# Performance work log

Hardware: AMD Instinct MI355X
Metric: run time of the kernel (lower is better)

Reference implementation:

```python
import jax, jax.numpy as jnp
import numpy as np

N = 200000          # nodes
G = 8192            # graphs (data.num_graphs)
NUM_RADIAL = 32
M_OUT = 85          # embedding_depth // 3 -> 85x1o


def setup_inputs() -> dict:
    key = jax.random.key(0)
    ks = jax.random.split(key, 24)
    f32 = jnp.float32
    def rn(k, shape, scale=1.0):
        return jax.random.normal(k, shape, dtype=f32) * scale
    inp = {}
    inp['pos'] = rn(ks[0], (N, 3))
    inp['z'] = jax.random.randint(ks[1], (N,), 0, 100)
    inp['batch'] = jnp.sort(jax.random.randint(ks[2], (N,), 0, G))
    inp['node_table'] = rn(ks[3], (100, 32))
    # MLP weights (fan-in scaled), biases zero
    inp['W_rbf0'] = rn(ks[4], (32, 64), 32 ** -0.5)
    inp['b_rbf0'] = jnp.zeros((64,), f32)
    inp['W_rbf1'] = rn(ks[5], (64, 64), 64 ** -0.5)
    inp['b_rbf1'] = jnp.zeros((64,), f32)
    inp['W_m0'] = rn(ks[6], (96, 64), 96 ** -0.5)
    inp['b_m0'] = jnp.zeros((64,), f32)
    inp['W_m1'] = rn(ks[7], (64, 64), 64 ** -0.5)
    inp['b_m1'] = jnp.zeros((64,), f32)
    inp['W_m2'] = rn(ks[8], (64, 64), 64 ** -0.5)
    inp['b_m2'] = jnp.zeros((64,), f32)
    # e3nn-style weights: N(0,1), path normalization applied in the math
    inp['w_tp0'] = rn(ks[9], (64, 64))   # 0e x 0e -> 0e
    inp['w_tp1'] = rn(ks[10], (64, 64))  # 0e x 1o -> 1o
    inp['w_tp2'] = rn(ks[11], (64, 32))  # 0e x 2e -> 2e
    inp['L0'] = rn(ks[12], (64, 64))     # o3.Linear 0e block
    inp['L1o'] = rn(ks[13], (64, 64))    # o3.Linear 1o block
    inp['L2e'] = rn(ks[14], (32, 32))    # o3.Linear 2e block
    inp['L_out'] = rn(ks[15], (64, 85))  # tl2: 64x1o -> 85x1o
    return inp


def _sph_harm(pos):
    # e3nn real spherical harmonics, normalize=False, normalization='component'
    x, y, z = pos[:, 0], pos[:, 1], pos[:, 2]
    sh0 = jnp.ones_like(x)                              # [N]     l=0
    sh1 = jnp.sqrt(3.0) * pos                           # [N,3]   l=1
    s15 = jnp.sqrt(15.0)
    s5 = jnp.sqrt(5.0)
    sh2 = jnp.stack([
        s15 * x * z,
        s15 * x * y,
        s5 * (y * y - 0.5 * (x * x + z * z)),
        s15 * y * z,
        0.5 * s15 * (z * z - x * x),
    ], axis=-1)                                          # [N,5]   l=2
    return sh0, sh1, sh2


def _forward(pos, z, batch, node_table, W_rbf0, b_rbf0, W_rbf1, b_rbf1,
             W_m0, b_m0, W_m1, b_m1, W_m2, b_m2,
             w_tp0, w_tp1, w_tp2, L0, L1o, L2e, L_out):
    sh0, sh1, sh2 = _sph_harm(pos)  # centroid is zeros

    # Gaussian RBF on |pos|, start=0 stop=1
    dist = jnp.linalg.norm(pos, axis=1)                  # [N]
    offsets = jnp.linspace(0.0, 1.0, NUM_RADIAL)
    coeff = -0.5 / (offsets[1] - offsets[0]) ** 2
    rbf = jnp.exp(coeff * (dist[:, None] - offsets) ** 2)  # [N,32]

    # rbf_emb MLP (1 hidden layer)
    r = jax.nn.gelu(rbf @ W_rbf0 + b_rbf0)
    r = r @ W_rbf1 + b_rbf1                               # [N,64]

    # radial_message MLP (2 hidden layers) on [r_emb, node_emb]
    h = jnp.concatenate([r, node_table[z]], axis=-1)      # [N,96]
    h = jax.nn.gelu(h @ W_m0 + b_m0)
    h = jax.nn.gelu(h @ W_m1 + b_m1)
    msg = h @ W_m2 + b_m2                                 # [N,64]  64x0e

    # FullyConnectedTensorProduct(64x0e, 1x0e+1x1o+1x2e -> irreps_mid)
    # scalar (x) l  -> l ; path norm 1/sqrt(fan_in), fan_in = 64*1
    inv = 1.0 / jnp.sqrt(64.0)
    c0 = (msg @ w_tp0) * sh0[:, None] * inv               # [N,64]    0e
    c1 = (msg @ w_tp1)[:, :, None] * sh1[:, None, :] * inv  # [N,64,3] 1o
    c2 = (msg @ w_tp2)[:, :, None] * sh2[:, None, :] * inv  # [N,32,5] 2e
    # 64x1e and 32x2o output blocks have no allowed paths -> identically zero

    # act1: gelu on scalar (0e) irreps only
    c0 = jax.nn.gelu(c0)

    # scatter mean + scatter sum over graphs
    cnt = jnp.maximum(jax.ops.segment_sum(jnp.ones_like(dist), batch, num_segments=G), 1.0)
    def agg(v, cshape):
        s = jax.ops.segment_sum(v, batch, num_segments=G)
        return s / cnt.reshape(cshape) + s
    g0 = agg(c0, (G, 1))        # [G,64]
    g1 = agg(c1, (G, 1, 1))     # [G,64,3]
    g2 = agg(c2, (G, 1, 1))     # [G,32,5]

    # tl1 (o3.Linear, per-irrep multiplicity mixing, 1/sqrt(mult_in) norm)
    g0 = g0 @ L0 * (64 ** -0.5)
    g1 = jnp.einsum('gum,uv->gvm', g1, L1o) * (64 ** -0.5)
    g2 = jnp.einsum('gum,uv->gvm', g2, L2e) * (32 ** -0.5)

    # act2: gelu on 0e only (g0 subsequently dropped by tl2's 1o-only output)
    g0 = jax.nn.gelu(g0)

    # tl2: irreps_mid -> 85x1o; only the 1o block contributes
    enc = jnp.einsum('gum,uv->gvm', g1, L_out) * (64 ** -0.5)  # [G,85,3]
    return enc.reshape(G, M_OUT * 3)


def reference(pos, z, batch, node_table, W_rbf0, b_rbf0, W_rbf1, b_rbf1,
              W_m0, b_m0, W_m1, b_m1, W_m2, b_m2,
              w_tp0, w_tp1, w_tp2, L0, L1o, L2e, L_out):
    return _forward(pos, z, batch, node_table, W_rbf0, b_rbf0, W_rbf1, b_rbf1,
                    W_m0, b_m0, W_m1, b_m1, W_m2, b_m2,
                    w_tp0, w_tp1, w_tp2, L0, L1o, L2e, L_out)
```

## Files before the change

kernel.cpp:

```cpp
#include <hip/hip_runtime.h>


typedef __attribute__((ext_vector_type(8))) short bf16x8;
typedef __attribute__((ext_vector_type(4))) float f32x4;
typedef unsigned short ushort_t;

#define SBW 72

__device__ __forceinline__ unsigned rnebits(float x) {
    unsigned u = __float_as_uint(x);
    return u + 0x7fffu + ((u >> 16) & 1u);
}
__device__ __forceinline__ ushort_t f2bf(float x) { return (ushort_t)(rnebits(x) >> 16); }
__device__ __forceinline__ float bf2f(ushort_t h) { return __uint_as_float(((unsigned)h) << 16); }
__device__ __forceinline__ unsigned pack2bf(float lo, float hi) {
    return (rnebits(hi) & 0xffff0000u) | (rnebits(lo) >> 16);
}
__device__ __forceinline__ void lds_fence() {
    asm volatile("s_waitcnt lgkmcnt(0)" ::: "memory");
    __builtin_amdgcn_sched_barrier(0);
}

__device__ __forceinline__ float gelu(float x) {
    float x2 = x * x;
    float y  = x * fmaf(0.10294324f, x2, 2.3022082f);
    float e  = __builtin_amdgcn_exp2f(y);
    float r  = __builtin_amdgcn_rcpf(e + 1.0f);
    return fmaf(-x, r, x);
}

__global__ __launch_bounds__(256)
void prep_kernel(const float* __restrict__ W_rbf0, const float* __restrict__ W_rbf1,
                 const float* __restrict__ W_m0, const float* __restrict__ W_m1,
                 const float* __restrict__ W_m2, const float* __restrict__ b_m2,
                 const float* __restrict__ w_tp1,
                 const float* __restrict__ L1o, const float* __restrict__ L_out,
                 const float* __restrict__ node_table, const int* __restrict__ batch,
                 ushort_t* __restrict__ wb, float* __restrict__ bc,
                 float* __restrict__ Lcomb, int* __restrict__ seg, int N, int G)
{
    if (blockIdx.x >= 115) {
        int i = (blockIdx.x - 115) * 256 + threadIdx.x;
        if (i >= N) return;
        int bi = batch[i];
        int bprev = (i == 0) ? -1 : batch[i - 1];
        for (int g = bprev + 1; g <= bi; ++g) seg[g] = i;
        if (i == N - 1) for (int g = bi + 1; g <= G; ++g) seg[g] = N;
        return;
    }
    int idx = blockIdx.x * 256 + threadIdx.x;
    float w;
    ushort_t *dh, *dl;
    if (idx < 2048) {
        int f = idx >> 5, k = idx & 31;
        w = W_rbf0[k * 64 + f]; dh = wb + idx; dl = wb + 2048 + idx;
    } else if (idx < 6144) {
        int j = idx - 2048, f = j >> 6, k = j & 63;
        w = W_rbf1[k * 64 + f]; dh = wb + 4096 + j; dl = wb + 8192 + j;
    } else if (idx < 12288) {
        int j = idx - 6144, f = j / 96, k = j - 96 * f;
        w = W_m0[k * 64 + f]; dh = wb + 12288 + j; dl = wb + 18432 + j;
    } else if (idx < 16384) {
        int j = idx - 12288, f = j >> 6, k = j & 63;
        w = W_m1[k * 64 + f]; dh = wb + 24576 + j; dl = wb + 28672 + j;
    } else if (idx < 20480) {
        int j = idx - 16384, f = j >> 6, k = j & 63;
        float s = 0.f;
        for (int jj = 0; jj < 64; ++jj) s = fmaf(W_m2[k * 64 + jj], w_tp1[jj * 64 + f], s);
        w = s; dh = wb + 32768 + j; dl = wb + 36864 + j;
    } else if (idx < 20544) {
        int b = idx - 20480;
        float s = 0.f;
        for (int k = 0; k < 64; ++k) s = fmaf(b_m2[k], w_tp1[k * 64 + b], s);
        bc[b] = s;
        return;
    } else if (idx < 25984) {
        int j = idx - 20544, u = j / 85, v = j - 85 * u;
        float s = 0.f;
        for (int k = 0; k < 64; ++k) s = fmaf(L1o[u * 64 + k], L_out[k * 85 + v], s);
        Lcomb[j] = 0.015625f * s;
        return;
    } else if (idx < 29184) {
        int j = idx - 25984;
        wb[40960 + j] = f2bf(node_table[j]);
        return;
    } else return;
    ushort_t h = f2bf(w);
    *dh = h;
    *dl = f2bf(w - bf2f(h));
}

template<int KT, int ACT, bool TABLE>
__device__ __forceinline__ void layerX(
    const ushort_t* __restrict__ Wh, const ushort_t* __restrict__ Wl,
    const float* __restrict__ bias,
    const ushort_t* src, ushort_t* dst,
    const ushort_t* __restrict__ tab_bf, const int* __restrict__ zp,
    int nodebase, int N, int lrow, int lcol)
{
    constexpr int K = TABLE ? (KT * 32 + 32) : (KT * 32);
    f32x4 acc[4][4];
    #pragma unroll
    for (int m = 0; m < 4; ++m) {
        float4 bv = *(const float4*)(bias + m * 16 + lrow * 4);
        #pragma unroll
        for (int n = 0; n < 4; ++n) {
            acc[m][n][0] = bv.x; acc[m][n][1] = bv.y; acc[m][n][2] = bv.z; acc[m][n][3] = bv.w;
        }
    }
    #pragma unroll
    for (int kt = 0; kt < KT; ++kt) {
        const int kof = kt * 32 + lrow * 8;
        bf16x8 bb[4];
        #pragma unroll
        for (int n = 0; n < 4; ++n)
            bb[n] = *(const bf16x8*)&src[(n * 16 + lcol) * SBW + kof];
        #pragma unroll
        for (int m = 0; m < 4; ++m) {
            bf16x8 ah = *(const bf16x8*)(Wh + (m * 16 + lcol) * K + kof);
            bf16x8 al = *(const bf16x8*)(Wl + (m * 16 + lcol) * K + kof);
            #pragma unroll
            for (int n = 0; n < 4; ++n) {
                acc[m][n] = __builtin_amdgcn_mfma_f32_16x16x32_bf16(ah, bb[n], acc[m][n], 0, 0, 0);
                acc[m][n] = __builtin_amdgcn_mfma_f32_16x16x32_bf16(al, bb[n], acc[m][n], 0, 0, 0);
            }
        }
    }
    if (TABLE) {
        const int kof = KT * 32 + lrow * 8;
        bf16x8 bb[4];
        #pragma unroll
        for (int n = 0; n < 4; ++n) {
            int node = nodebase + n * 16 + lcol;
            if (node > N - 1) node = N - 1;
            bb[n] = *(const bf16x8*)(tab_bf + zp[node] * 32 + lrow * 8);
        }
        #pragma unroll
        for (int m = 0; m < 4; ++m) {
            bf16x8 ah = *(const bf16x8*)(Wh + (m * 16 + lcol) * K + kof);
            bf16x8 al = *(const bf16x8*)(Wl + (m * 16 + lcol) * K + kof);
            #pragma unroll
            for (int n = 0; n < 4; ++n) {
                acc[m][n] = __builtin_amdgcn_mfma_f32_16x16x32_bf16(ah, bb[n], acc[m][n], 0, 0, 0);
                acc[m][n] = __builtin_amdgcn_mfma_f32_16x16x32_bf16(al, bb[n], acc[m][n], 0, 0, 0);
            }
        }
    }
    #pragma unroll
    for (int m = 0; m < 4; ++m) {
        const int f0 = m * 16 + lrow * 4;
        #pragma unroll
        for (int n = 0; n < 4; ++n) {
            f32x4 v = acc[m][n];
            if (ACT == 1) {
                #pragma unroll
                for (int r = 0; r < 4; ++r) v[r] = gelu(v[r]);
            }
            uint2 pk;
            pk.x = pack2bf(v[0], v[1]);
            pk.y = pack2bf(v[2], v[3]);
            *(uint2*)&dst[(n * 16 + lcol) * SBW + f0] = pk;
        }
    }
}

__global__ __launch_bounds__(64, 2)
void node_mfma_kernel(const float* __restrict__ pos, const int* __restrict__ z,
                      const ushort_t* __restrict__ wb,
                      const float* __restrict__ b_rbf0, const float* __restrict__ b_rbf1,
                      const float* __restrict__ b_m0, const float* __restrict__ b_m1,
                      const float* __restrict__ bc,
                      ushort_t* __restrict__ Tout, int N)
{
    __shared__ ushort_t bufA[64 * SBW];
    __shared__ ushort_t bufB[64 * SBW];
    const int lane = threadIdx.x;
    const int nodebase = blockIdx.x * 64;
    int gn = nodebase + lane;
    if (gn >= N) gn = N - 1;
    const ushort_t* tab_bf = wb + 40960;

    {
        const float px = pos[3 * gn], py = pos[3 * gn + 1], pz = pos[3 * gn + 2];
        const float dist = sqrtf(px * px + py * py + pz * pz);
        unsigned rb[16];
        #pragma unroll
        for (int j = 0; j < 16; ++j) {
            float d0 = dist - (float)(2 * j)     * (1.0f / 31.0f);
            float d1 = dist - (float)(2 * j + 1) * (1.0f / 31.0f);
            rb[j] = pack2bf(__builtin_amdgcn_exp2f(-693.2149671554846f * d0 * d0),
                            __builtin_amdgcn_exp2f(-693.2149671554846f * d1 * d1));
        }
        uint4* dst = (uint4*)&bufA[lane * SBW];
        dst[0] = make_uint4(rb[0], rb[1], rb[2], rb[3]);
        dst[1] = make_uint4(rb[4], rb[5], rb[6], rb[7]);
        dst[2] = make_uint4(rb[8], rb[9], rb[10], rb[11]);
        dst[3] = make_uint4(rb[12], rb[13], rb[14], rb[15]);
    }
    lds_fence();

    const int lrow = lane >> 4, lcol = lane & 15;
    layerX<1, 1, false>(wb + 0, wb + 2048, b_rbf0, bufA, bufB, tab_bf, z, nodebase, N, lrow, lcol);
    lds_fence();
    layerX<2, 0, false>(wb + 4096, wb + 8192, b_rbf1, bufB, bufA, tab_bf, z, nodebase, N, lrow, lcol);
    lds_fence();
    layerX<2, 1, true>(wb + 12288, wb + 18432, b_m0, bufA, bufB, tab_bf, z, nodebase, N, lrow, lcol);
    lds_fence();
    layerX<2, 1, false>(wb + 24576, wb + 28672, b_m1, bufB, bufA, tab_bf, z, nodebase, N, lrow, lcol);
    lds_fence();
    layerX<2, 0, false>(wb + 32768, wb + 36864, bc, bufA, bufB, tab_bf, z, nodebase, N, lrow, lcol);
    lds_fence();

    {
        ushort_t* tb = Tout + (size_t)nodebase * 64;
        #pragma unroll
        for (int i = 0; i < 8; ++i) {
            bf16x8 v = *(const bf16x8*)&bufB[(i * 8 + (lane >> 3)) * SBW + (lane & 7) * 8];
            *(bf16x8*)(tb + i * 512 + lane * 8) = v;
        }
    }
}

__global__ __launch_bounds__(256)
void graph_kernel(const ushort_t* __restrict__ Tin, const float* __restrict__ pos,
                  const int* __restrict__ seg, const float* __restrict__ Lcomb,
                  float* __restrict__ out, int G) {
    __shared__ float g1s[4][64][3];
    const int lane = threadIdx.x & 63;
    const int wid = threadIdx.x >> 6;
    const int g = blockIdx.x * 4 + wid;
    const bool active = g < G;

    if (active) {
        const int s = seg[g], e = seg[g + 1];
        float a0 = 0.f, a1 = 0.f, a2 = 0.f;
        for (int nn = s; nn < e; ++nn) {
            float t = bf2f(Tin[(size_t)nn * 64 + lane]);
            float qx = pos[3 * nn + 0], qy = pos[3 * nn + 1], qz = pos[3 * nn + 2];
            a0 = fmaf(t, qx, a0);
            a1 = fmaf(t, qy, a1);
            a2 = fmaf(t, qz, a2);
        }
        float cnt = (float)((e - s) > 0 ? (e - s) : 1);
        float sc = 1.7320508075688772f * 0.125f * (1.0f + 1.0f / cnt);
        g1s[wid][lane][0] = a0 * sc;
        g1s[wid][lane][1] = a1 * sc;
        g1s[wid][lane][2] = a2 * sc;
    }
    __syncthreads();
    if (!active) return;

    float o0 = 0.f, o1 = 0.f, o2 = 0.f, p0 = 0.f, p1 = 0.f, p2 = 0.f;
    const int v2 = 64 + lane;
    for (int u = 0; u < 64; ++u) {
        float b0 = g1s[wid][u][0], b1 = g1s[wid][u][1], b2 = g1s[wid][u][2];
        float l0 = Lcomb[u * 85 + lane];
        o0 = fmaf(b0, l0, o0); o1 = fmaf(b1, l0, o1); o2 = fmaf(b2, l0, o2);
        if (lane < 21) {
            float l1 = Lcomb[u * 85 + v2];
            p0 = fmaf(b0, l1, p0); p1 = fmaf(b1, l1, p1); p2 = fmaf(b2, l1, p2);
        }
    }
    float* og = out + (size_t)g * 255;
    og[3 * lane + 0] = o0; og[3 * lane + 1] = o1; og[3 * lane + 2] = o2;
    if (lane < 21) {
        og[3 * v2 + 0] = p0; og[3 * v2 + 1] = p1; og[3 * v2 + 2] = p2;
    }
}

extern "C" void kernel_launch(void* const* d_in, const int* in_sizes, int n_in,
                              void* d_out, int out_size, void* d_ws, size_t ws_size,
                              hipStream_t stream) {
    const float* pos        = (const float*)d_in[0];
    const int*   z          = (const int*)d_in[1];
    const int*   batch      = (const int*)d_in[2];
    const float* node_table = (const float*)d_in[3];
    const float* W_rbf0     = (const float*)d_in[4];
    const float* b_rbf0     = (const float*)d_in[5];
    const float* W_rbf1     = (const float*)d_in[6];
    const float* b_rbf1     = (const float*)d_in[7];
    const float* W_m0       = (const float*)d_in[8];
    const float* b_m0       = (const float*)d_in[9];
    const float* W_m1       = (const float*)d_in[10];
    const float* b_m1       = (const float*)d_in[11];
    const float* W_m2       = (const float*)d_in[12];
    const float* b_m2       = (const float*)d_in[13];
    const float* w_tp1      = (const float*)d_in[15];
    const float* L1o        = (const float*)d_in[18];
    const float* L_out      = (const float*)d_in[20];
    float* out = (float*)d_out;

    const int N = in_sizes[0] / 3;
    const int G = out_size / 255;

    char* ws = (char*)d_ws;
    float*    bc    = (float*)(ws + 0);
    float*    Lcomb = (float*)(ws + 256);
    int*      seg   = (int*)(ws + 22528);
    ushort_t* wb    = (ushort_t*)(ws + 55552);
    ushort_t* T     = (ushort_t*)(ws + 144128);

    const int segBlocks = (N + 255) / 256;
    prep_kernel<<<115 + segBlocks, 256, 0, stream>>>(
        W_rbf0, W_rbf1, W_m0, W_m1, W_m2, b_m2, w_tp1, L1o, L_out,
        node_table, batch, wb, bc, Lcomb, seg, N, G);

    node_mfma_kernel<<<(N + 63) / 64, 64, 0, stream>>>(
        pos, z, wb, b_rbf0, b_rbf1, b_m0, b_m1, bc, T, N);

    graph_kernel<<<(G + 3) / 4, 256, 0, stream>>>(T, pos, seg, Lcomb, out, G);
}
```

Measured before the change: 81.63 us.

## Make node MLP kernel persistent with register-resident weights and single LDS buffer

Turns the node MLP kernel into a persistent grid-stride kernel of up to 1024 single-wave blocks. The layer 2–5 hi/lo bf16 weight fragments are loaded into registers once per block instead of being re-read for every 64-node tile. The two LDS ping-pong buffers become one in-place buffer, and the waitcnt fences are replaced by scheduling barriers. pack2bf now uses a byte-permute instruction. This raises register pressure (launch bounds drop to 1 wave per SIMD) and relies on the compiler's own waitcnt insertion to keep LDS ordering correct.

After: 99.14 us. +21.5%, slower.

```diff
diff --git a/kernel.cpp b/kernel.cpp
--- a/kernel.cpp
+++ b/kernel.cpp
@@ -13,12 +13,17 @@
 }
 __device__ __forceinline__ ushort_t f2bf(float x) { return (ushort_t)(rnebits(x) >> 16); }
 __device__ __forceinline__ float bf2f(ushort_t h) { return __uint_as_float(((unsigned)h) << 16); }
+#if __has_builtin(__builtin_amdgcn_perm)
+__device__ __forceinline__ unsigned pack2bf(float lo, float hi) {
+    return __builtin_amdgcn_perm(rnebits(hi), rnebits(lo), 0x07060302u);
+}
+#else
 __device__ __forceinline__ unsigned pack2bf(float lo, float hi) {
     return (rnebits(hi) & 0xffff0000u) | (rnebits(lo) >> 16);
 }
-__device__ __forceinline__ void lds_fence() {
-    asm volatile("s_waitcnt lgkmcnt(0)" ::: "memory");
-    __builtin_amdgcn_sched_barrier(0);
+#endif
+__device__ __forceinline__ void ds_order_fence() {
+    __builtin_amdgcn_sched_barrier(0x7F);
 }
 
 __device__ __forceinline__ float gelu(float x) {
@@ -90,62 +95,8 @@
     *dl = f2bf(w - bf2f(h));
 }
 
-template<int KT, int ACT, bool TABLE>
-__device__ __forceinline__ void layerX(
-    const ushort_t* __restrict__ Wh, const ushort_t* __restrict__ Wl,
-    const float* __restrict__ bias,
-    const ushort_t* src, ushort_t* dst,
-    const ushort_t* __restrict__ tab_bf, const int* __restrict__ zp,
-    int nodebase, int N, int lrow, int lcol)
-{
-    constexpr int K = TABLE ? (KT * 32 + 32) : (KT * 32);
-    f32x4 acc[4][4];
-    #pragma unroll
-    for (int m = 0; m < 4; ++m) {
-        float4 bv = *(const float4*)(bias + m * 16 + lrow * 4);
-        #pragma unroll
-        for (int n = 0; n < 4; ++n) {
-            acc[m][n][0] = bv.x; acc[m][n][1] = bv.y; acc[m][n][2] = bv.z; acc[m][n][3] = bv.w;
-        }
-    }
-    #pragma unroll
-    for (int kt = 0; kt < KT; ++kt) {
-        const int kof = kt * 32 + lrow * 8;
-        bf16x8 bb[4];
-        #pragma unroll
-        for (int n = 0; n < 4; ++n)
-            bb[n] = *(const bf16x8*)&src[(n * 16 + lcol) * SBW + kof];
-        #pragma unroll
-        for (int m = 0; m < 4; ++m) {
-            bf16x8 ah = *(const bf16x8*)(Wh + (m * 16 + lcol) * K + kof);
-            bf16x8 al = *(const bf16x8*)(Wl + (m * 16 + lcol) * K + kof);
-            #pragma unroll
-            for (int n = 0; n < 4; ++n) {
-                acc[m][n] = __builtin_amdgcn_mfma_f32_16x16x32_bf16(ah, bb[n], acc[m][n], 0, 0, 0);
-                acc[m][n] = __builtin_amdgcn_mfma_f32_16x16x32_bf16(al, bb[n], acc[m][n], 0, 0, 0);
-            }
-        }
-    }
-    if (TABLE) {
-        const int kof = KT * 32 + lrow * 8;
-        bf16x8 bb[4];
-        #pragma unroll
-        for (int n = 0; n < 4; ++n) {
-            int node = nodebase + n * 16 + lcol;
-            if (node > N - 1) node = N - 1;
-            bb[n] = *(const bf16x8*)(tab_bf + zp[node] * 32 + lrow * 8);
-        }
-        #pragma unroll
-        for (int m = 0; m < 4; ++m) {
-            bf16x8 ah = *(const bf16x8*)(Wh + (m * 16 + lcol) * K + kof);
-            bf16x8 al = *(const bf16x8*)(Wl + (m * 16 + lcol) * K + kof);
-            #pragma unroll
-            for (int n = 0; n < 4; ++n) {
-                acc[m][n] = __builtin_amdgcn_mfma_f32_16x16x32_bf16(ah, bb[n], acc[m][n], 0, 0, 0);
-                acc[m][n] = __builtin_amdgcn_mfma_f32_16x16x32_bf16(al, bb[n], acc[m][n], 0, 0, 0);
-            }
-        }
-    }
+template<int ACT>
+__device__ __forceinline__ void epilogueR(f32x4 (&acc)[4][4], ushort_t* buf, int lrow, int lcol) {
     #pragma unroll
     for (int m = 0; m < 4; ++m) {
         const int f0 = m * 16 + lrow * 4;
@@ -159,65 +110,192 @@
             uint2 pk;
             pk.x = pack2bf(v[0], v[1]);
             pk.y = pack2bf(v[2], v[3]);
-            *(uint2*)&dst[(n * 16 + lcol) * SBW + f0] = pk;
-        }
-    }
-}
-
-__global__ __launch_bounds__(64, 2)
+            *(uint2*)&buf[(n * 16 + lcol) * SBW + f0] = pk;
+        }
+    }
+}
+
+template<int KT>
+__device__ __forceinline__ void accInit(f32x4 (&acc)[4][4], const float* __restrict__ bias,
+                                        int lrow) {
+    #pragma unroll
+    for (int m = 0; m < 4; ++m) {
+        float4 bv = *(const float4*)(bias + m * 16 + lrow * 4);
+        #pragma unroll
+        for (int n = 0; n < 4; ++n) {
+            acc[m][n][0] = bv.x; acc[m][n][1] = bv.y; acc[m][n][2] = bv.z; acc[m][n][3] = bv.w;
+        }
+    }
+    (void)0;
+}
+
+template<int KT>
+__device__ __forceinline__ void loadBB(bf16x8 (&bb)[4 * KT], const ushort_t* buf,
+                                       int lrow, int lcol) {
+    #pragma unroll
+    for (int n = 0; n < 4; ++n)
+        #pragma unroll
+        for (int kt = 0; kt < KT; ++kt)
+            bb[n * KT + kt] = *(const bf16x8*)&buf[(n * 16 + lcol) * SBW + kt * 32 + lrow * 8];
+}
+
+template<int KT>
+__device__ __forceinline__ void mfmaHL(f32x4 (&acc)[4][4], const bf16x8 (&wh)[4 * KT],
+                                       const bf16x8 (&wl)[4 * KT], const bf16x8 (&bb)[4 * KT]) {
+    #pragma unroll
+    for (int kt = 0; kt < KT; ++kt)
+        #pragma unroll
+        for (int m = 0; m < 4; ++m)
+            #pragma unroll
+            for (int n = 0; n < 4; ++n) {
+                acc[m][n] = __builtin_amdgcn_mfma_f32_16x16x32_bf16(wh[m * KT + kt], bb[n * KT + kt], acc[m][n], 0, 0, 0);
+                acc[m][n] = __builtin_amdgcn_mfma_f32_16x16x32_bf16(wl[m * KT + kt], bb[n * KT + kt], acc[m][n], 0, 0, 0);
+            }
+}
+
+__global__ __launch_bounds__(64, 1)
 void node_mfma_kernel(const float* __restrict__ pos, const int* __restrict__ z,
                       const ushort_t* __restrict__ wb,
                       const float* __restrict__ b_rbf0, const float* __restrict__ b_rbf1,
                       const float* __restrict__ b_m0, const float* __restrict__ b_m1,
                       const float* __restrict__ bc,
-                      ushort_t* __restrict__ Tout, int N)
+                      ushort_t* __restrict__ Tout, int N, int ntiles)
 {
-    __shared__ ushort_t bufA[64 * SBW];
-    __shared__ ushort_t bufB[64 * SBW];
+    __shared__ ushort_t buf[64 * SBW];
     const int lane = threadIdx.x;
-    const int nodebase = blockIdx.x * 64;
-    int gn = nodebase + lane;
-    if (gn >= N) gn = N - 1;
+    const int lrow = lane >> 4, lcol = lane & 15;
     const ushort_t* tab_bf = wb + 40960;
 
-    {
-        const float px = pos[3 * gn], py = pos[3 * gn + 1], pz = pos[3 * gn + 2];
-        const float dist = sqrtf(px * px + py * py + pz * pz);
-        unsigned rb[16];
-        #pragma unroll
-        for (int j = 0; j < 16; ++j) {
-            float d0 = dist - (float)(2 * j)     * (1.0f / 31.0f);
-            float d1 = dist - (float)(2 * j + 1) * (1.0f / 31.0f);
-            rb[j] = pack2bf(__builtin_amdgcn_exp2f(-693.2149671554846f * d0 * d0),
-                            __builtin_amdgcn_exp2f(-693.2149671554846f * d1 * d1));
-        }
-        uint4* dst = (uint4*)&bufA[lane * SBW];
-        dst[0] = make_uint4(rb[0], rb[1], rb[2], rb[3]);
-        dst[1] = make_uint4(rb[4], rb[5], rb[6], rb[7]);
-        dst[2] = make_uint4(rb[8], rb[9], rb[10], rb[11]);
-        dst[3] = make_uint4(rb[12], rb[13], rb[14], rb[15]);
-    }
-    lds_fence();
-
-    const int lrow = lane >> 4, lcol = lane & 15;
-    layerX<1, 1, false>(wb + 0, wb + 2048, b_rbf0, bufA, bufB, tab_bf, z, nodebase, N, lrow, lcol);
-    lds_fence();
-    layerX<2, 0, false>(wb + 4096, wb + 8192, b_rbf1, bufB, bufA, tab_bf, z, nodebase, N, lrow, lcol);
-    lds_fence();
-    layerX<2, 1, true>(wb + 12288, wb + 18432, b_m0, bufA, bufB, tab_bf, z, nodebase, N, lrow, lcol);
-    lds_fence();
-    layerX<2, 1, false>(wb + 24576, wb + 28672, b_m1, bufB, bufA, tab_bf, z, nodebase, N, lrow, lcol);
-    lds_fence();
-    layerX<2, 0, false>(wb + 32768, wb + 36864, bc, bufA, bufB, tab_bf, z, nodebase, N, lrow, lcol);
-    lds_fence();
-
-    {
-        ushort_t* tb = Tout + (size_t)nodebase * 64;
-        #pragma unroll
-        for (int i = 0; i < 8; ++i) {
-            bf16x8 v = *(const bf16x8*)&bufB[(i * 8 + (lane >> 3)) * SBW + (lane & 7) * 8];
-            *(bf16x8*)(tb + i * 512 + lane * 8) = v;
-        }
+    bf16x8 w2h[8], w2l[8], w3h[8], w3l[8], w4h[8], w4l[8], w5h[8], w5l[8];
+    #pragma unroll
+    for (int m = 0; m < 4; ++m)
+        #pragma unroll
+        for (int kt = 0; kt < 2; ++kt) {
+            const int i  = m * 2 + kt;
+            const int o  = (m * 16 + lcol) * 64 + kt * 32 + lrow * 8;
+            const int o3 = (m * 16 + lcol) * 96 + kt * 32 + lrow * 8;
+            w2h[i] = *(const bf16x8*)(wb + 4096  + o);
+            w2l[i] = *(const bf16x8*)(wb + 8192  + o);
+            w3h[i] = *(const bf16x8*)(wb + 12288 + o3);
+            w3l[i] = *(const bf16x8*)(wb + 18432 + o3);
+            w4h[i] = *(const bf16x8*)(wb + 24576 + o);
+            w4l[i] = *(const bf16x8*)(wb + 28672 + o);
+            w5h[i] = *(const bf16x8*)(wb + 32768 + o);
+            w5l[i] = *(const bf16x8*)(wb + 36864 + o);
+        }
+
+    for (int tile = blockIdx.x; tile < ntiles; tile += gridDim.x) {
+        const int nodebase = tile * 64;
+        int gn = nodebase + lane;
+        if (gn > N - 1) gn = N - 1;
+
+        {
+            const float px = pos[3 * gn], py = pos[3 * gn + 1], pz = pos[3 * gn + 2];
+            const float dist = sqrtf(px * px + py * py + pz * pz);
+            unsigned rb[16];
+            #pragma unroll
+            for (int j = 0; j < 16; ++j) {
+                float d0 = dist - (float)(2 * j)     * (1.0f / 31.0f);
+                float d1 = dist - (float)(2 * j + 1) * (1.0f / 31.0f);
+                rb[j] = pack2bf(__builtin_amdgcn_exp2f(-693.2149671554846f * d0 * d0),
+                                __builtin_amdgcn_exp2f(-693.2149671554846f * d1 * d1));
+            }
+            uint4* dst = (uint4*)&buf[lane * SBW];
+            dst[0] = make_uint4(rb[0], rb[1], rb[2], rb[3]);
+            dst[1] = make_uint4(rb[4], rb[5], rb[6], rb[7]);
+            dst[2] = make_uint4(rb[8], rb[9], rb[10], rb[11]);
+            dst[3] = make_uint4(rb[12], rb[13], rb[14], rb[15]);
+        }
+        ds_order_fence();
+
+        f32x4 acc[4][4];
+
+        {
+            bf16x8 w1h[4], w1l[4], bb[4];
+            #pragma unroll
+            for (int m = 0; m < 4; ++m) {
+                const int o = (m * 16 + lcol) * 32 + lrow * 8;
+                w1h[m] = *(const bf16x8*)(wb + 0    + o);
+                w1l[m] = *(const bf16x8*)(wb + 2048 + o);
+            }
+            accInit<1>(acc, b_rbf0, lrow);
+            loadBB<1>(bb, buf, lrow, lcol);
+            mfmaHL<1>(acc, w1h, w1l, bb);
+            ds_order_fence();
+            epilogueR<1>(acc, buf, lrow, lcol);
+        }
+        ds_order_fence();
+
+        {
+            bf16x8 bb[8];
+            accInit<2>(acc, b_rbf1, lrow);
+            loadBB<2>(bb, buf, lrow, lcol);
+            mfmaHL<2>(acc, w2h, w2l, bb);
+            ds_order_fence();
+            epilogueR<0>(acc, buf, lrow, lcol);
+        }
+        ds_order_fence();
+
+        {
+            bf16x8 bb[8], th[4], tl[4], tb[4];
+            #pragma unroll
+            for (int m = 0; m < 4; ++m) {
+                const int o3 = (m * 16 + lcol) * 96 + 64 + lrow * 8;
+                th[m] = *(const bf16x8*)(wb + 12288 + o3);
+                tl[m] = *(const bf16x8*)(wb + 18432 + o3);
+            }
+            #pragma unroll
+            for (int n = 0; n < 4; ++n) {
+                int node = nodebase + n * 16 + lcol;
+                if (node > N - 1) node = N - 1;
+                tb[n] = *(const bf16x8*)(tab_bf + z[node] * 32 + lrow * 8);
+            }
+            accInit<2>(acc, b_m0, lrow);
+            loadBB<2>(bb, buf, lrow, lcol);
+            mfmaHL<2>(acc, w3h, w3l, bb);
+            #pragma unroll
+            for (int m = 0; m < 4; ++m)
+                #pragma unroll
+                for (int n = 0; n < 4; ++n) {
+                    acc[m][n] = __builtin_amdgcn_mfma_f32_16x16x32_bf16(th[m], tb[n], acc[m][n], 0, 0, 0);
+                    acc[m][n] = __builtin_amdgcn_mfma_f32_16x16x32_bf16(tl[m], tb[n], acc[m][n], 0, 0, 0);
+                }
+            ds_order_fence();
+            epilogueR<1>(acc, buf, lrow, lcol);
+        }
+        ds_order_fence();
+
+        {
+            bf16x8 bb[8];
+            accInit<2>(acc, b_m1, lrow);
+            loadBB<2>(bb, buf, lrow, lcol);
+            mfmaHL<2>(acc, w4h, w4l, bb);
+            ds_order_fence();
+            epilogueR<1>(acc, buf, lrow, lcol);
+        }
+        ds_order_fence();
+
+        {
+            bf16x8 bb[8];
+            accInit<2>(acc, bc, lrow);
+            loadBB<2>(bb, buf, lrow, lcol);
+            mfmaHL<2>(acc, w5h, w5l, bb);
+            ds_order_fence();
+            epilogueR<0>(acc, buf, lrow, lcol);
+        }
+        ds_order_fence();
+
+        {
+            ushort_t* tb2 = Tout + (size_t)nodebase * 64;
+            #pragma unroll
+            for (int i = 0; i < 8; ++i) {
+                const int r = i * 8 + (lane >> 3);
+                bf16x8 v = *(const bf16x8*)&buf[r * SBW + (lane & 7) * 8];
+                if (nodebase + r < N)
+                    *(bf16x8*)(tb2 + i * 512 + lane * 8) = v;
+            }
+        }
+        ds_order_fence();
     }
 }
 
@@ -292,6 +370,7 @@
 
     const int N = in_sizes[0] / 3;
     const int G = out_size / 255;
+    const int ntiles = (N + 63) / 64;
 
     char* ws = (char*)d_ws;
     float*    bc    = (float*)(ws + 0);
@@ -305,8 +384,9 @@
         W_rbf0, W_rbf1, W_m0, W_m1, W_m2, b_m2, w_tp1, L1o, L_out,
         node_table, batch, wb, bc, Lcomb, seg, N, G);
 
-    node_mfma_kernel<<<(N + 63) / 64, 64, 0, stream>>>(
-        pos, z, wb, b_rbf0, b_rbf1, b_m0, b_m1, bc, T, N);
+    const int nodeBlocks = ntiles < 1024 ? ntiles : 1024;
+    node_mfma_kernel<<<nodeBlocks, 64, 0, stream>>>(
+        pos, z, wb, b_rbf0, b_rbf1, b_m0, b_m1, bc, T, N, ntiles);
 
     graph_kernel<<<(G + 3) / 4, 256, 0, stream>>>(T, pos, seg, Lcomb, out, G);
 }
```

## Fold node embedding table into layer bias and unify MLP layers in one buffer

Applied to the files above, without the earlier changes.

Precomputes node_table·W_m0[64:96]+b_m0 per atom type in prep, so the third layer starts its accumulators from a gathered per-node bias and skips the extra K=32 table MFMA pass. All five layers are padded to K=64 and run in a non-unrolled loop over one LDS buffer, which cuts code size and LDS use, and occupancy is raised to 4 waves per block slot. The lgkmcnt wait fences are replaced with scheduling barriers only, which relies on in-order LDS execution within a single wave. The first layer now does extra MFMAs on zero padding, and the T output store gains a bounds guard.

Result: slower. 88.20 us (+8.0%).

```diff
diff --git a/kernel.cpp b/kernel.cpp
--- a/kernel.cpp
+++ b/kernel.cpp
@@ -16,9 +16,8 @@
 __device__ __forceinline__ unsigned pack2bf(float lo, float hi) {
     return (rnebits(hi) & 0xffff0000u) | (rnebits(lo) >> 16);
 }
-__device__ __forceinline__ void lds_fence() {
-    asm volatile("s_waitcnt lgkmcnt(0)" ::: "memory");
-    __builtin_amdgcn_sched_barrier(0);
+__device__ __forceinline__ void ds_order_fence() {
+    __builtin_amdgcn_sched_barrier(0x7F);
 }
 
 __device__ __forceinline__ float gelu(float x) {
@@ -32,15 +31,16 @@
 __global__ __launch_bounds__(256)
 void prep_kernel(const float* __restrict__ W_rbf0, const float* __restrict__ W_rbf1,
                  const float* __restrict__ W_m0, const float* __restrict__ W_m1,
-                 const float* __restrict__ W_m2, const float* __restrict__ b_m2,
-                 const float* __restrict__ w_tp1,
+                 const float* __restrict__ W_m2, const float* __restrict__ b_m0,
+                 const float* __restrict__ b_m2, const float* __restrict__ w_tp1,
                  const float* __restrict__ L1o, const float* __restrict__ L_out,
                  const float* __restrict__ node_table, const int* __restrict__ batch,
-                 ushort_t* __restrict__ wb, float* __restrict__ bc,
-                 float* __restrict__ Lcomb, int* __restrict__ seg, int N, int G)
+                 ushort_t* __restrict__ wb, float* __restrict__ tblc,
+                 float* __restrict__ bc, float* __restrict__ Lcomb,
+                 int* __restrict__ seg, int N, int G)
 {
-    if (blockIdx.x >= 115) {
-        int i = (blockIdx.x - 115) * 256 + threadIdx.x;
+    if (blockIdx.x >= 127) {
+        int i = (blockIdx.x - 127) * 256 + threadIdx.x;
         if (i >= N) return;
         int bi = batch[i];
         int bprev = (i == 0) ? -1 : batch[i - 1];
@@ -51,15 +51,16 @@
     int idx = blockIdx.x * 256 + threadIdx.x;
     float w;
     ushort_t *dh, *dl;
-    if (idx < 2048) {
-        int f = idx >> 5, k = idx & 31;
-        w = W_rbf0[k * 64 + f]; dh = wb + idx; dl = wb + 2048 + idx;
-    } else if (idx < 6144) {
-        int j = idx - 2048, f = j >> 6, k = j & 63;
-        w = W_rbf1[k * 64 + f]; dh = wb + 4096 + j; dl = wb + 8192 + j;
+    if (idx < 4096) {
+        int f = idx >> 6, k = idx & 63;
+        w = (k < 32) ? W_rbf0[k * 64 + f] : 0.0f;
+        dh = wb + idx; dl = wb + 4096 + idx;
+    } else if (idx < 8192) {
+        int j = idx - 4096, f = j >> 6, k = j & 63;
+        w = W_rbf1[k * 64 + f]; dh = wb + 8192 + j; dl = wb + 12288 + j;
     } else if (idx < 12288) {
-        int j = idx - 6144, f = j / 96, k = j - 96 * f;
-        w = W_m0[k * 64 + f]; dh = wb + 12288 + j; dl = wb + 18432 + j;
+        int j = idx - 8192, f = j >> 6, k = j & 63;
+        w = W_m0[k * 64 + f]; dh = wb + 16384 + j; dl = wb + 20480 + j;
     } else if (idx < 16384) {
         int j = idx - 12288, f = j >> 6, k = j & 63;
         w = W_m1[k * 64 + f]; dh = wb + 24576 + j; dl = wb + 28672 + j;
@@ -68,21 +69,23 @@
         float s = 0.f;
         for (int jj = 0; jj < 64; ++jj) s = fmaf(W_m2[k * 64 + jj], w_tp1[jj * 64 + f], s);
         w = s; dh = wb + 32768 + j; dl = wb + 36864 + j;
-    } else if (idx < 20544) {
-        int b = idx - 20480;
+    } else if (idx < 26880) {
+        int j = idx - 20480, zz = j >> 6, f = j & 63;
+        float s = b_m0[f];
+        for (int k = 0; k < 32; ++k) s = fmaf(node_table[zz * 32 + k], W_m0[(64 + k) * 64 + f], s);
+        tblc[j] = s;
+        return;
+    } else if (idx < 26944) {
+        int b = idx - 26880;
         float s = 0.f;
         for (int k = 0; k < 64; ++k) s = fmaf(b_m2[k], w_tp1[k * 64 + b], s);
         bc[b] = s;
         return;
-    } else if (idx < 25984) {
-        int j = idx - 20544, u = j / 85, v = j - 85 * u;
+    } else if (idx < 32384) {
+        int j = idx - 26944, u = j / 85, v = j - 85 * u;
         float s = 0.f;
         for (int k = 0; k < 64; ++k) s = fmaf(L1o[u * 64 + k], L_out[k * 85 + v], s);
         Lcomb[j] = 0.015625f * s;
-        return;
-    } else if (idx < 29184) {
-        int j = idx - 25984;
-        wb[40960 + j] = f2bf(node_table[j]);
         return;
     } else return;
     ushort_t h = f2bf(w);
@@ -90,95 +93,20 @@
     *dl = f2bf(w - bf2f(h));
 }
 
-template<int KT, int ACT, bool TABLE>
-__device__ __forceinline__ void layerX(
-    const ushort_t* __restrict__ Wh, const ushort_t* __restrict__ Wl,
-    const float* __restrict__ bias,
-    const ushort_t* src, ushort_t* dst,
-    const ushort_t* __restrict__ tab_bf, const int* __restrict__ zp,
-    int nodebase, int N, int lrow, int lcol)
-{
-    constexpr int K = TABLE ? (KT * 32 + 32) : (KT * 32);
-    f32x4 acc[4][4];
-    #pragma unroll
-    for (int m = 0; m < 4; ++m) {
-        float4 bv = *(const float4*)(bias + m * 16 + lrow * 4);
-        #pragma unroll
-        for (int n = 0; n < 4; ++n) {
-            acc[m][n][0] = bv.x; acc[m][n][1] = bv.y; acc[m][n][2] = bv.z; acc[m][n][3] = bv.w;
-        }
-    }
-    #pragma unroll
-    for (int kt = 0; kt < KT; ++kt) {
-        const int kof = kt * 32 + lrow * 8;
-        bf16x8 bb[4];
-        #pragma unroll
-        for (int n = 0; n < 4; ++n)
-            bb[n] = *(const bf16x8*)&src[(n * 16 + lcol) * SBW + kof];
-        #pragma unroll
-        for (int m = 0; m < 4; ++m) {
-            bf16x8 ah = *(const bf16x8*)(Wh + (m * 16 + lcol) * K + kof);
-            bf16x8 al = *(const bf16x8*)(Wl + (m * 16 + lcol) * K + kof);
-            #pragma unroll
-            for (int n = 0; n < 4; ++n) {
-                acc[m][n] = __builtin_amdgcn_mfma_f32_16x16x32_bf16(ah, bb[n], acc[m][n], 0, 0, 0);
-                acc[m][n] = __builtin_amdgcn_mfma_f32_16x16x32_bf16(al, bb[n], acc[m][n], 0, 0, 0);
-            }
-        }
-    }
-    if (TABLE) {
-        const int kof = KT * 32 + lrow * 8;
-        bf16x8 bb[4];
-        #pragma unroll
-        for (int n = 0; n < 4; ++n) {
-            int node = nodebase + n * 16 + lcol;
-            if (node > N - 1) node = N - 1;
-            bb[n] = *(const bf16x8*)(tab_bf + zp[node] * 32 + lrow * 8);
-        }
-        #pragma unroll
-        for (int m = 0; m < 4; ++m) {
-            bf16x8 ah = *(const bf16x8*)(Wh + (m * 16 + lcol) * K + kof);
-            bf16x8 al = *(const bf16x8*)(Wl + (m * 16 + lcol) * K + kof);
-            #pragma unroll
-            for (int n = 0; n < 4; ++n) {
-                acc[m][n] = __builtin_amdgcn_mfma_f32_16x16x32_bf16(ah, bb[n], acc[m][n], 0, 0, 0);
-                acc[m][n] = __builtin_amdgcn_mfma_f32_16x16x32_bf16(al, bb[n], acc[m][n], 0, 0, 0);
-            }
-        }
-    }
-    #pragma unroll
-    for (int m = 0; m < 4; ++m) {
-        const int f0 = m * 16 + lrow * 4;
-        #pragma unroll
-        for (int n = 0; n < 4; ++n) {
-            f32x4 v = acc[m][n];
-            if (ACT == 1) {
-                #pragma unroll
-                for (int r = 0; r < 4; ++r) v[r] = gelu(v[r]);
-            }
-            uint2 pk;
-            pk.x = pack2bf(v[0], v[1]);
-            pk.y = pack2bf(v[2], v[3]);
-            *(uint2*)&dst[(n * 16 + lcol) * SBW + f0] = pk;
-        }
-    }
-}
-
-__global__ __launch_bounds__(64, 2)
+__global__ __launch_bounds__(64, 4)
 void node_mfma_kernel(const float* __restrict__ pos, const int* __restrict__ z,
                       const ushort_t* __restrict__ wb,
+                      const float* __restrict__ tblc,
                       const float* __restrict__ b_rbf0, const float* __restrict__ b_rbf1,
-                      const float* __restrict__ b_m0, const float* __restrict__ b_m1,
-                      const float* __restrict__ bc,
+                      const float* __restrict__ b_m1, const float* __restrict__ bc,
                       ushort_t* __restrict__ Tout, int N)
 {
-    __shared__ ushort_t bufA[64 * SBW];
-    __shared__ ushort_t bufB[64 * SBW];
+    __shared__ ushort_t buf[64 * SBW];
     const int lane = threadIdx.x;
+    const int lrow = lane >> 4, lcol = lane & 15;
     const int nodebase = blockIdx.x * 64;
     int gn = nodebase + lane;
-    if (gn >= N) gn = N - 1;
-    const ushort_t* tab_bf = wb + 40960;
+    if (gn > N - 1) gn = N - 1;
 
     {
         const float px = pos[3 * gn], py = pos[3 * gn + 1], pz = pos[3 * gn + 2];
@@ -191,32 +119,109 @@
             rb[j] = pack2bf(__builtin_amdgcn_exp2f(-693.2149671554846f * d0 * d0),
                             __builtin_amdgcn_exp2f(-693.2149671554846f * d1 * d1));
         }
-        uint4* dst = (uint4*)&bufA[lane * SBW];
+        uint4* dst = (uint4*)&buf[lane * SBW];
         dst[0] = make_uint4(rb[0], rb[1], rb[2], rb[3]);
         dst[1] = make_uint4(rb[4], rb[5], rb[6], rb[7]);
         dst[2] = make_uint4(rb[8], rb[9], rb[10], rb[11]);
         dst[3] = make_uint4(rb[12], rb[13], rb[14], rb[15]);
-    }
-    lds_fence();
-
-    const int lrow = lane >> 4, lcol = lane & 15;
-    layerX<1, 1, false>(wb + 0, wb + 2048, b_rbf0, bufA, bufB, tab_bf, z, nodebase, N, lrow, lcol);
-    lds_fence();
-    layerX<2, 0, false>(wb + 4096, wb + 8192, b_rbf1, bufB, bufA, tab_bf, z, nodebase, N, lrow, lcol);
-    lds_fence();
-    layerX<2, 1, true>(wb + 12288, wb + 18432, b_m0, bufA, bufB, tab_bf, z, nodebase, N, lrow, lcol);
-    lds_fence();
-    layerX<2, 1, false>(wb + 24576, wb + 28672, b_m1, bufB, bufA, tab_bf, z, nodebase, N, lrow, lcol);
-    lds_fence();
-    layerX<2, 0, false>(wb + 32768, wb + 36864, bc, bufA, bufB, tab_bf, z, nodebase, N, lrow, lcol);
-    lds_fence();
-
+        uint4 zz = make_uint4(0, 0, 0, 0);
+        dst[4] = zz; dst[5] = zz; dst[6] = zz; dst[7] = zz;
+    }
+    int zn0, zn1, zn2, zn3;
     {
-        ushort_t* tb = Tout + (size_t)nodebase * 64;
+        int n0 = nodebase + 0  + lcol; if (n0 > N - 1) n0 = N - 1;
+        int n1 = nodebase + 16 + lcol; if (n1 > N - 1) n1 = N - 1;
+        int n2 = nodebase + 32 + lcol; if (n2 > N - 1) n2 = N - 1;
+        int n3 = nodebase + 48 + lcol; if (n3 > N - 1) n3 = N - 1;
+        zn0 = z[n0]; zn1 = z[n1]; zn2 = z[n2]; zn3 = z[n3];
+    }
+    ds_order_fence();
+
+    #pragma unroll 1
+    for (int L = 0; L < 5; ++L) {
+        const ushort_t* whb = wb + L * 8192;
+        f32x4 acc[4][4];
+        if (L == 2) {
+            const int zn[4] = {zn0, zn1, zn2, zn3};
+            #pragma unroll
+            for (int n = 0; n < 4; ++n) {
+                const float* tp = tblc + zn[n] * 64 + lrow * 4;
+                #pragma unroll
+                for (int m = 0; m < 4; ++m) {
+                    float4 bv = *(const float4*)(tp + m * 16);
+                    acc[m][n][0] = bv.x; acc[m][n][1] = bv.y;
+                    acc[m][n][2] = bv.z; acc[m][n][3] = bv.w;
+                }
+            }
+        } else {
+            const float* bp = (L == 0) ? b_rbf0 : (L == 1) ? b_rbf1 : (L == 3) ? b_m1 : bc;
+            #pragma unroll
+            for (int m = 0; m < 4; ++m) {
+                float4 bv = *(const float4*)(bp + m * 16 + lrow * 4);
+                #pragma unroll
+                for (int n = 0; n < 4; ++n) {
+                    acc[m][n][0] = bv.x; acc[m][n][1] = bv.y;
+                    acc[m][n][2] = bv.z; acc[m][n][3] = bv.w;
+                }
+            }
+        }
+        #pragma unroll
+        for (int kt = 0; kt < 2; ++kt) {
+            const int kof = kt * 32 + lrow * 8;
+            bf16x8 bb[4];
+            #pragma unroll
+            for (int n = 0; n < 4; ++n)
+                bb[n] = *(const bf16x8*)&buf[(n * 16 + lcol) * SBW + kof];
+            #pragma unroll
+            for (int m = 0; m < 4; ++m) {
+                bf16x8 ah = *(const bf16x8*)(whb + (m * 16 + lcol) * 64 + kof);
+                bf16x8 al = *(const bf16x8*)(whb + 4096 + (m * 16 + lcol) * 64 + kof);
+                #pragma unroll
+                for (int n = 0; n < 4; ++n) {
+                    acc[m][n] = __builtin_amdgcn_mfma_f32_16x16x32_bf16(ah, bb[n], acc[m][n], 0, 0, 0);
+                    acc[m][n] = __builtin_amdgcn_mfma_f32_16x16x32_bf16(al, bb[n], acc[m][n], 0, 0, 0);
+                }
+            }
+        }
+        ds_order_fence();
+        if ((L == 0) | (L == 2) | (L == 3)) {
+            #pragma unroll
+            for (int m = 0; m < 4; ++m) {
+                const int f0 = m * 16 + lrow * 4;
+                #pragma unroll
+                for (int n = 0; n < 4; ++n) {
+                    f32x4 v = acc[m][n];
+                    uint2 pk;
+                    pk.x = pack2bf(gelu(v[0]), gelu(v[1]));
+                    pk.y = pack2bf(gelu(v[2]), gelu(v[3]));
+                    *(uint2*)&buf[(n * 16 + lcol) * SBW + f0] = pk;
+                }
+            }
+        } else {
+            #pragma unroll
+            for (int m = 0; m < 4; ++m) {
+                const int f0 = m * 16 + lrow * 4;
+                #pragma unroll
+                for (int n = 0; n < 4; ++n) {
+                    f32x4 v = acc[m][n];
+                    uint2 pk;
+                    pk.x = pack2bf(v[0], v[1]);
+                    pk.y = pack2bf(v[2], v[3]);
+                    *(uint2*)&buf[(n * 16 + lcol) * SBW + f0] = pk;
+                }
+            }
+        }
+        ds_order_fence();
+    }
+
+    {
+        ushort_t* tb2 = Tout + (size_t)nodebase * 64;
         #pragma unroll
         for (int i = 0; i < 8; ++i) {
-            bf16x8 v = *(const bf16x8*)&bufB[(i * 8 + (lane >> 3)) * SBW + (lane & 7) * 8];
-            *(bf16x8*)(tb + i * 512 + lane * 8) = v;
+            const int r = i * 8 + (lane >> 3);
+            bf16x8 v = *(const bf16x8*)&buf[r * SBW + (lane & 7) * 8];
+            if (nodebase + r < N)
+                *(bf16x8*)(tb2 + i * 512 + lane * 8) = v;
         }
     }
 }
@@ -292,21 +297,23 @@
 
     const int N = in_sizes[0] / 3;
     const int G = out_size / 255;
+    const int ntiles = (N + 63) / 64;
 
     char* ws = (char*)d_ws;
     float*    bc    = (float*)(ws + 0);
     float*    Lcomb = (float*)(ws + 256);
     int*      seg   = (int*)(ws + 22528);
     ushort_t* wb    = (ushort_t*)(ws + 55552);
-    ushort_t* T     = (ushort_t*)(ws + 144128);
+    float*    tblc  = (float*)(ws + 137472);
+    ushort_t* T     = (ushort_t*)(ws + 163072);
 
     const int segBlocks = (N + 255) / 256;
-    prep_kernel<<<115 + segBlocks, 256, 0, stream>>>(
-        W_rbf0, W_rbf1, W_m0, W_m1, W_m2, b_m2, w_tp1, L1o, L_out,
-        node_table, batch, wb, bc, Lcomb, seg, N, G);
-
-    node_mfma_kernel<<<(N + 63) / 64, 64, 0, stream>>>(
-        pos, z, wb, b_rbf0, b_rbf1, b_m0, b_m1, bc, T, N);
+    prep_kernel<<<127 + segBlocks, 256, 0, stream>>>(
+        W_rbf0, W_rbf1, W_m0, W_m1, W_m2, b_m0, b_m2, w_tp1, L1o, L_out,
+        node_table, batch, wb, tblc, bc, Lcomb, seg, N, G);
+
+    node_mfma_kernel<<<ntiles, 64, 0, stream>>>(
+        pos, z, wb, tblc, b_rbf0, b_rbf1, b_m1, bc, T, N);
 
     graph_kernel<<<(G + 3) / 4, 256, 0, stream>>>(T, pos, seg, Lcomb, out, G);
 }
```
